# Kernel tuning notes

Hardware: AMD Instinct MI355X
Metric: run time of the kernel (lower is better)

The kernel has to match this reference:

```python
import jax, jax.numpy as jnp
import numpy as np

B, S, DM = 2, 2048, 2048
H, KV, HD = 32, 8, 64
ROPE_BASE = 10000.0


def rotate_half(x):
    x1, x2 = jnp.split(x, 2, axis=-1)
    return jnp.concatenate([-x2, x1], axis=-1)


def setup_inputs() -> dict:
    key = jax.random.key(0)
    ks = jax.random.split(key, 8)
    hidden_states = jax.random.normal(ks[0], (B, S, DM), dtype=jnp.float32)
    attention_mask = jnp.ones((B, S), dtype=jnp.int32)
    # RoPE tables: inv_freq over half the head dim, duplicated (HF-style)
    inv_freq = 1.0 / (ROPE_BASE ** (jnp.arange(0, HD, 2, dtype=jnp.float32) / HD))
    pos = jnp.arange(S, dtype=jnp.float32)
    freqs = pos[:, None] * inv_freq[None, :]            # [S, HD/2]
    emb = jnp.concatenate([freqs, freqs], axis=-1)      # [S, HD]
    cos = jnp.broadcast_to(jnp.cos(emb)[None], (B, S, HD))
    sin = jnp.broadcast_to(jnp.sin(emb)[None], (B, S, HD))
    sc = 1.0 / np.sqrt(DM)
    W_q = jax.random.normal(ks[1], (DM, H * HD), dtype=jnp.float32) * sc
    W_k = jax.random.normal(ks[2], (DM, KV * HD), dtype=jnp.float32) * sc
    W_v = jax.random.normal(ks[3], (DM, KV * HD), dtype=jnp.float32) * sc
    b_v = jax.random.normal(ks[4], (KV * HD,), dtype=jnp.float32) * 0.01
    W_o = jax.random.normal(ks[5], (H * HD, DM), dtype=jnp.float32) * sc
    b_o = jax.random.normal(ks[6], (DM,), dtype=jnp.float32) * 0.01
    return {"hidden_states": hidden_states, "attention_mask": attention_mask,
            "cos": cos, "sin": sin, "W_q": W_q, "W_k": W_k, "W_v": W_v,
            "b_v": b_v, "W_o": W_o, "b_o": b_o}


def reference(hidden_states, attention_mask, cos, sin, W_q, W_k, W_v, b_v, W_o, b_o):
    b, s, _ = hidden_states.shape
    q = hidden_states @ W_q                       # [B,S,H*HD]
    k = hidden_states @ W_k                       # [B,S,KV*HD]
    v = hidden_states @ W_v + b_v                 # [B,S,KV*HD]
    q = q.reshape(b, s, H, HD).transpose(0, 2, 1, 3)    # [B,H,S,HD]
    k = k.reshape(b, s, KV, HD).transpose(0, 2, 1, 3)   # [B,KV,S,HD]
    v = v.reshape(b, s, KV, HD).transpose(0, 2, 1, 3)
    c = cos[:, None]                              # [B,1,S,HD]
    sn = sin[:, None]
    q = q * c + rotate_half(q) * sn
    k = k * c + rotate_half(k) * sn
    groups = H // KV
    k = jnp.repeat(k, groups, axis=1)             # [B,H,S,HD]
    v = jnp.repeat(v, groups, axis=1)
    A = jnp.einsum('bhqd,bhkd->bhqk', q, k) / np.sqrt(HD).astype(np.float32)
    neg_inf = jnp.float32(-jnp.inf)
    causal = jnp.triu(jnp.full((s, s), neg_inf, dtype=jnp.float32), k=1)[None, None]
    mask = jnp.where(attention_mask[:, None, None, :] == 0, neg_inf, causal)
    A = jax.nn.softmax(A + mask, axis=-1)
    o = jnp.einsum('bhqk,bhkd->bhqd', A, v)
    o = o.transpose(0, 2, 1, 3).reshape(b, s, H * HD)
    return o @ W_o + b_o
```

## Files before the change

### kernel.cpp

```cpp
#include <hip/hip_runtime.h>
#include <hip/hip_bf16.h>

#define Bb 2
#define Ss 2048
#define DMD 2048
#define Hh 32
#define KVh 8
#define HD 64

using bf16 = __hip_bfloat16;
typedef __attribute__((ext_vector_type(8))) short short8;
typedef __attribute__((ext_vector_type(4))) float floatx4;

__device__ inline float tof(const bf16 x) { return __bfloat162float(x); }
__device__ inline void stor(float* p, float v) { *p = v; }
__device__ inline void stor(bf16* p, float v) { *p = __float2bfloat16(v); }
__device__ inline short bf16bits(float v) {
    union { bf16 h; short s; } cv; cv.h = __float2bfloat16(v); return cv.s;
}

__device__ inline void gl_lds16(const bf16* g, bf16* l) {
    __builtin_amdgcn_global_load_lds(
        (const __attribute__((address_space(1))) unsigned int*)g,
        (__attribute__((address_space(3))) unsigned int*)l, 16, 0, 0);
}

__global__ __launch_bounds__(256) void cvt_bf16_kernel(
    const float* __restrict__ in, bf16* __restrict__ out, int total8)
{
    const int i = blockIdx.x * 256 + threadIdx.x;
    if (i >= total8) return;
    const float4 a = ((const float4*)in)[2 * i];
    const float4 b = ((const float4*)in)[2 * i + 1];
    short8 r;
    r[0] = bf16bits(a.x); r[1] = bf16bits(a.y); r[2] = bf16bits(a.z); r[3] = bf16bits(a.w);
    r[4] = bf16bits(b.x); r[5] = bf16bits(b.y); r[6] = bf16bits(b.z); r[7] = bf16bits(b.w);
    ((short8*)out)[i] = r;
}

__global__ __launch_bounds__(256) void cvtT_kernel(
    const float* __restrict__ W, bf16* __restrict__ Wt,
    int N, int K, int rowOff)
{
    __shared__ float t[32][33];
    const int n0 = blockIdx.x * 32;
    const int k0 = blockIdx.y * 32;
    const int tx = threadIdx.x & 31, ty = threadIdx.x >> 5;
    #pragma unroll
    for (int r = 0; r < 32; r += 8)
        t[ty + r][tx] = W[(size_t)(k0 + ty + r) * N + n0 + tx];
    __syncthreads();
    #pragma unroll
    for (int r = 0; r < 32; r += 8)
        Wt[(size_t)(rowOff + n0 + ty + r) * K + k0 + tx] =
            __float2bfloat16(t[tx][ty + r]);
}

template <int EPI>
__global__ __launch_bounds__(256) void gemm_bt(
    const bf16* __restrict__ A, const bf16* __restrict__ Bt,
    const float* __restrict__ bias,
    bf16* __restrict__ Yq, bf16* __restrict__ Yk, bf16* __restrict__ Yv,
    float* __restrict__ Yo, int M, int N, int K)
{
    __shared__ bf16 As[128 * 32];
    __shared__ bf16 Bs[128 * 32];

    const int tid  = threadIdx.x;
    const int wave = tid >> 6, lane = tid & 63;
    const int lid  = lane & 15, quad = lane >> 4;
    const int wr = (wave >> 1) * 64, wc = (wave & 1) * 64;
    const size_t bm = (size_t)blockIdx.y * 128, bn = (size_t)blockIdx.x * 128;

    floatx4 acc[4][4];
    #pragma unroll
    for (int i = 0; i < 4; ++i)
        #pragma unroll
        for (int j = 0; j < 4; ++j)
            acc[i][j] = (floatx4){0.f, 0.f, 0.f, 0.f};

    for (int k0 = 0; k0 < K; k0 += 32) {
        #pragma unroll
        for (int i = 0; i < 2; ++i) {
            const int c   = wave * 128 + i * 64 + lane;
            const int row = c >> 2, col = (c & 3) * 8;
            gl_lds16(A  + (bm + row) * (size_t)K + k0 + col,
                     &As[(wave * 128 + i * 64) * 8]);
            gl_lds16(Bt + (bn + row) * (size_t)K + k0 + col,
                     &Bs[(wave * 128 + i * 64) * 8]);
        }
        __syncthreads();

        short8 af[4], bfr[4];
        #pragma unroll
        for (int i = 0; i < 4; ++i)
            af[i] = *(const short8*)&As[(wr + i * 16 + lid) * 32 + quad * 8];
        #pragma unroll
        for (int j = 0; j < 4; ++j)
            bfr[j] = *(const short8*)&Bs[(wc + j * 16 + lid) * 32 + quad * 8];
        #pragma unroll
        for (int i = 0; i < 4; ++i)
            #pragma unroll
            for (int j = 0; j < 4; ++j)
                acc[i][j] = __builtin_amdgcn_mfma_f32_16x16x32_bf16(
                    af[i], bfr[j], acc[i][j], 0, 0, 0);
        __syncthreads();
    }

    #pragma unroll
    for (int i = 0; i < 4; ++i) {
        const int gm0 = (int)bm + wr + i * 16 + quad * 4;
        #pragma unroll
        for (int j = 0; j < 4; ++j) {
            const int gn = (int)bn + wc + j * 16 + lid;
            #pragma unroll
            for (int r = 0; r < 4; ++r) {
                float v = acc[i][j][r];
                const int gm = gm0 + r;
                if (EPI == 0) {
                    if (gn < Hh * HD) {
                        stor(&Yq[(size_t)gm * (Hh * HD) + gn], v);
                    } else if (gn < Hh * HD + KVh * HD) {
                        stor(&Yk[(size_t)gm * (KVh * HD) + (gn - Hh * HD)], v);
                    } else {
                        const int c = gn - (Hh * HD + KVh * HD);
                        v += bias[c];
                        const int kvh = c >> 6, dd = c & 63;
                        const int bbi = gm >> 11, s = gm & (Ss - 1);
                        stor(&Yv[(((size_t)bbi * KVh + kvh) * HD + dd) * Ss + s], v);
                    }
                } else {
                    Yo[(size_t)gm * N + gn] = v + bias[gn];
                }
            }
        }
    }
}

__global__ void rope_kernel(bf16* __restrict__ buf,
                            const float* __restrict__ cosb,
                            const float* __restrict__ sinb,
                            int nheads, int total, float scale)
{
    int idx = blockIdx.x * blockDim.x + threadIdx.x;
    if (idx >= total) return;
    int d = idx & 31;
    int h = (idx >> 5) % nheads;
    int bs = idx / (32 * nheads);
    bf16* row = buf + ((size_t)bs * nheads + h) * HD;
    float x1 = tof(row[d]), x2 = tof(row[d + 32]);
    float c1 = cosb[(size_t)bs * HD + d];
    float s1 = sinb[(size_t)bs * HD + d];
    float c2 = cosb[(size_t)bs * HD + d + 32];
    float s2 = sinb[(size_t)bs * HD + d + 32];
    stor(&row[d],      (x1 * c1 - x2 * s1) * scale);
    stor(&row[d + 32], (x2 * c2 + x1 * s2) * scale);
}

template <bool CAUSAL>
__device__ inline void fattn_tile(
    const int k0, const int m0,
    const bf16* __restrict__ kBase, const bf16* __restrict__ vBase,
    const int* __restrict__ mBase,
    const short8 qf0[2], const short8 qf1[2],
    floatx4 o[2][4], float lsum[2][4],
    short (*pw)[16][72],
    const int lid, const int quad)
{
    const size_t kStride = (size_t)KVh * HD;

    short8 kb0[4], kb1[4];
    #pragma unroll
    for (int nt = 0; nt < 4; ++nt) {
        const bf16* kr = kBase + (size_t)(k0 + nt * 16 + lid) * kStride + quad * 8;
        kb0[nt] = *(const short8*)(kr);
        kb1[nt] = *(const short8*)(kr + 32);
    }
    floatx4 s[2][4];
    __builtin_amdgcn_s_setprio(1);
    #pragma unroll
    for (int nt = 0; nt < 4; ++nt)
        #pragma unroll
        for (int g = 0; g < 2; ++g) {
            floatx4 c = (floatx4){0.f, 0.f, 0.f, 0.f};
            c = __builtin_amdgcn_mfma_f32_16x16x32_bf16(qf0[g], kb0[nt], c, 0, 0, 0);
            c = __builtin_amdgcn_mfma_f32_16x16x32_bf16(qf1[g], kb1[nt], c, 0, 0, 0);
            s[g][nt] = c;
        }
    __builtin_amdgcn_s_setprio(0);

    short8 vb0[4], vb1[4];
    #pragma unroll
    for (int nt = 0; nt < 4; ++nt) {
        const bf16* vr = vBase + (size_t)(nt * 16 + lid) * Ss + k0 + quad * 8;
        vb0[nt] = *(const short8*)(vr);
        vb1[nt] = *(const short8*)(vr + 32);
    }

    #pragma unroll
    for (int nt = 0; nt < 4; ++nt) {
        const int col = k0 + nt * 16 + lid;
        const int mk  = mBase[col];
        #pragma unroll
        for (int g = 0; g < 2; ++g) {
            const int mr0 = m0 + g * 16 + quad * 4;
            #pragma unroll
            for (int rr = 0; rr < 4; ++rr) {
                float p;
                if (CAUSAL)
                    p = (mk == 0 || col > mr0 + rr) ? 0.f : __expf(s[g][nt][rr]);
                else
                    p = (mk == 0) ? 0.f : __expf(s[g][nt][rr]);
                s[g][nt][rr] = p;
                lsum[g][rr] += p;
            }
        }
    }

    #pragma unroll
    for (int g = 0; g < 2; ++g)
        #pragma unroll
        for (int nt = 0; nt < 4; ++nt)
            #pragma unroll
            for (int rr = 0; rr < 4; ++rr)
                pw[g][quad * 4 + rr][nt * 16 + lid] = bf16bits(s[g][nt][rr]);
    short8 pf0[2], pf1[2];
    #pragma unroll
    for (int g = 0; g < 2; ++g) {
        pf0[g] = *(const short8*)&pw[g][lid][quad * 8];
        pf1[g] = *(const short8*)&pw[g][lid][32 + quad * 8];
    }

    __builtin_amdgcn_s_setprio(1);
    #pragma unroll
    for (int nt = 0; nt < 4; ++nt)
        #pragma unroll
        for (int g = 0; g < 2; ++g) {
            o[g][nt] = __builtin_amdgcn_mfma_f32_16x16x32_bf16(
                pf0[g], vb0[nt], o[g][nt], 0, 0, 0);
            o[g][nt] = __builtin_amdgcn_mfma_f32_16x16x32_bf16(
                pf1[g], vb1[nt], o[g][nt], 0, 0, 0);
        }
    __builtin_amdgcn_s_setprio(0);
}

__global__ __launch_bounds__(256) void fattn_kernel(
    bf16* __restrict__ QO, const bf16* __restrict__ Kb,
    const bf16* __restrict__ Vt, const int* __restrict__ mask)
{
    const int bid    = blockIdx.x;
    const int kvh    = bid & 7;
    const int rest   = bid >> 3;
    const int qbslot = rest >> 3;
    const int bh     = rest & 7;
    const int hg     = bh & 3;
    const int b      = bh >> 2;
    const int qb     = 15 - qbslot;
    const int h      = kvh * 4 + hg;

    const int tid  = threadIdx.x;
    const int wave = tid >> 6;
    const int lane = tid & 63;
    const int lid  = lane & 15;
    const int quad = lane >> 4;

    const int qw = qb * 4 + wave;
    const int m0 = qw * 32;
    const int nfull = qw >> 1;

    __shared__ short pLds[4][2][16][72];

    const size_t kStride = (size_t)KVh * HD;
    const bf16* kBase = Kb + ((size_t)b * Ss) * kStride + (size_t)kvh * HD;
    const bf16* vBase = Vt + ((size_t)(b * KVh + kvh) * HD) * Ss;
    const int*  mBase = mask + b * Ss;

    short8 qf0[2], qf1[2];
    #pragma unroll
    for (int g = 0; g < 2; ++g) {
        const bf16* qb_ = QO + ((size_t)(b * Ss + m0 + g * 16 + lid) * Hh + h) * HD
                        + quad * 8;
        qf0[g] = *(const short8*)(qb_);
        qf1[g] = *(const short8*)(qb_ + 32);
    }

    floatx4 o[2][4];
    float lsum[2][4];
    #pragma unroll
    for (int g = 0; g < 2; ++g) {
        #pragma unroll
        for (int nt = 0; nt < 4; ++nt) o[g][nt] = (floatx4){0.f, 0.f, 0.f, 0.f};
        #pragma unroll
        for (int rr = 0; rr < 4; ++rr) lsum[g][rr] = 0.f;
    }

    for (int kt = 0; kt < nfull; ++kt)
        fattn_tile<false>(kt * 64, m0, kBase, vBase, mBase,
                          qf0, qf1, o, lsum, pLds[wave], lid, quad);
    fattn_tile<true>(nfull * 64, m0, kBase, vBase, mBase,
                     qf0, qf1, o, lsum, pLds[wave], lid, quad);

    #pragma unroll
    for (int g = 0; g < 2; ++g)
        #pragma unroll
        for (int rr = 0; rr < 4; ++rr) {
            float rs = lsum[g][rr];
            rs += __shfl_xor(rs, 1);
            rs += __shfl_xor(rs, 2);
            rs += __shfl_xor(rs, 4);
            rs += __shfl_xor(rs, 8);
            const float inv = 1.f / rs;
            const int m = m0 + g * 16 + quad * 4 + rr;
            bf16* orow = QO + ((size_t)(b * Ss + m) * Hh + h) * HD;
            #pragma unroll
            for (int nt = 0; nt < 4; ++nt)
                stor(&orow[nt * 16 + lid], o[g][nt][rr] * inv);
        }
}

extern "C" void kernel_launch(void* const* d_in, const int* in_sizes, int n_in,
                              void* d_out, int out_size, void* d_ws, size_t ws_size,
                              hipStream_t stream)
{
    const float* hs   = (const float*)d_in[0];
    const int*   mask = (const int*)d_in[1];
    const float* cosb = (const float*)d_in[2];
    const float* sinb = (const float*)d_in[3];
    const float* Wq   = (const float*)d_in[4];
    const float* Wk   = (const float*)d_in[5];
    const float* Wv   = (const float*)d_in[6];
    const float* bv   = (const float*)d_in[7];
    const float* Wo   = (const float*)d_in[8];
    const float* bo   = (const float*)d_in[9];
    float* out = (float*)d_out;

    const int M = Bb * Ss;

    bf16* QO    = (bf16*)d_ws;
    bf16* Wqkvt = QO + (size_t)M * (Hh * HD);
    bf16* Wot   = Wqkvt + (size_t)3072 * DMD;

    bf16* Kb  = (bf16*)d_out;
    bf16* Vt  = Kb + (size_t)M * (KVh * HD);
    bf16* Abf = Vt + (size_t)M * (KVh * HD);

    dim3 blk(256);

    const int total8 = M * DMD / 8;
    cvt_bf16_kernel<<<(total8 + 255) / 256, blk, 0, stream>>>(hs, Abf, total8);
    cvtT_kernel<<<dim3((Hh * HD) / 32, DMD / 32), blk, 0, stream>>>(
        Wq, Wqkvt, Hh * HD, DMD, 0);
    cvtT_kernel<<<dim3((KVh * HD) / 32, DMD / 32), blk, 0, stream>>>(
        Wk, Wqkvt, KVh * HD, DMD, Hh * HD);
    cvtT_kernel<<<dim3((KVh * HD) / 32, DMD / 32), blk, 0, stream>>>(
        Wv, Wqkvt, KVh * HD, DMD, Hh * HD + KVh * HD);
    cvtT_kernel<<<dim3(DMD / 32, DMD / 32), blk, 0, stream>>>(
        Wo, Wot, DMD, DMD, 0);

    gemm_bt<0><<<dim3(3072 / 128, M / 128), blk, 0, stream>>>(
        Abf, Wqkvt, bv, QO, Kb, Vt, nullptr, M, 3072, DMD);

    int totq = M * Hh * 32, totk = M * KVh * 32;
    rope_kernel<<<(totq + 255) / 256, blk, 0, stream>>>(QO, cosb, sinb, Hh, totq, 0.125f);
    rope_kernel<<<(totk + 255) / 256, blk, 0, stream>>>(Kb, cosb, sinb, KVh, totk, 1.0f);

    fattn_kernel<<<dim3(1024), blk, 0, stream>>>(QO, Kb, Vt, mask);

    gemm_bt<1><<<dim3(DMD / 128, M / 128), blk, 0, stream>>>(
        QO, Wot, bo, nullptr, nullptr, nullptr, out, M, DMD, DMD);
}
```

Baseline: 411.4 us.

## Compute transposed S tile and move P into MFMA layout with ds_permute instead of LDS

The QK^T MFMA now computes S transposed (K as the A operand), so each lane holds scores for one query row. The P tile is then converted with packed bf16 conversion and rearranged into the PV MFMA operand layout through ds_permute lane shuffles, replacing the LDS store/load round trip and the shared-memory buffer. Mask values are loaded as int4 vectors and row sums become per-lane, reducing the final shuffle count. The permute mapping is subtle and a mistake would silently corrupt results, and ds_permute still uses LDS hardware bandwidth.

```diff
diff --git a/kernel.cpp b/kernel.cpp
--- a/kernel.cpp
+++ b/kernel.cpp
@@ -17,6 +17,12 @@
 __device__ inline void stor(bf16* p, float v) { *p = __float2bfloat16(v); }
 __device__ inline short bf16bits(float v) {
     union { bf16 h; short s; } cv; cv.h = __float2bfloat16(v); return cv.s;
+}
+
+__device__ inline unsigned cvtpk_bf16(float lo, float hi) {
+    unsigned r;
+    asm("v_cvt_pk_bf16_f32 %0, %1, %2" : "=v"(r) : "v"(lo), "v"(hi));
+    return r;
 }
 
 __device__ inline void gl_lds16(const bf16* g, bf16* l) {
@@ -158,90 +164,96 @@
 }
 
 template <bool CAUSAL>
-__device__ inline void fattn_tile(
+__device__ __forceinline__ void fattn_tile(
     const int k0, const int m0,
     const bf16* __restrict__ kBase, const bf16* __restrict__ vBase,
     const int* __restrict__ mBase,
     const short8 qf0[2], const short8 qf1[2],
-    floatx4 o[2][4], float lsum[2][4],
-    short (*pw)[16][72],
-    const int lid, const int quad)
+    floatx4 o[2][4], float lsum[2],
+    const int lid, const int quad,
+    const int dstA[2], const int dstB[2])
 {
     const size_t kStride = (size_t)KVh * HD;
 
-    short8 kb0[4], kb1[4];
+    short8 ka0[4], ka1[4];
     #pragma unroll
     for (int nt = 0; nt < 4; ++nt) {
         const bf16* kr = kBase + (size_t)(k0 + nt * 16 + lid) * kStride + quad * 8;
-        kb0[nt] = *(const short8*)(kr);
-        kb1[nt] = *(const short8*)(kr + 32);
-    }
-    floatx4 s[2][4];
+        ka0[nt] = *(const short8*)(kr);
+        ka1[nt] = *(const short8*)(kr + 32);
+    }
+
+    floatx4 st[2][4];
     __builtin_amdgcn_s_setprio(1);
     #pragma unroll
     for (int nt = 0; nt < 4; ++nt)
         #pragma unroll
         for (int g = 0; g < 2; ++g) {
             floatx4 c = (floatx4){0.f, 0.f, 0.f, 0.f};
-            c = __builtin_amdgcn_mfma_f32_16x16x32_bf16(qf0[g], kb0[nt], c, 0, 0, 0);
-            c = __builtin_amdgcn_mfma_f32_16x16x32_bf16(qf1[g], kb1[nt], c, 0, 0, 0);
-            s[g][nt] = c;
+            c = __builtin_amdgcn_mfma_f32_16x16x32_bf16(ka0[nt], qf0[g], c, 0, 0, 0);
+            c = __builtin_amdgcn_mfma_f32_16x16x32_bf16(ka1[nt], qf1[g], c, 0, 0, 0);
+            st[g][nt] = c;
         }
     __builtin_amdgcn_s_setprio(0);
 
-    short8 vb0[4], vb1[4];
+    short8 vb[4][2];
+    #pragma unroll
+    for (int dt = 0; dt < 4; ++dt)
+        #pragma unroll
+        for (int ch = 0; ch < 2; ++ch)
+            vb[dt][ch] = *(const short8*)(vBase + (size_t)(dt * 16 + lid) * Ss
+                                          + k0 + ch * 32 + quad * 8);
+
+    int mk[4][4];
     #pragma unroll
     for (int nt = 0; nt < 4; ++nt) {
-        const bf16* vr = vBase + (size_t)(nt * 16 + lid) * Ss + k0 + quad * 8;
-        vb0[nt] = *(const short8*)(vr);
-        vb1[nt] = *(const short8*)(vr + 32);
-    }
-
-    #pragma unroll
-    for (int nt = 0; nt < 4; ++nt) {
-        const int col = k0 + nt * 16 + lid;
-        const int mk  = mBase[col];
-        #pragma unroll
-        for (int g = 0; g < 2; ++g) {
-            const int mr0 = m0 + g * 16 + quad * 4;
-            #pragma unroll
-            for (int rr = 0; rr < 4; ++rr) {
-                float p;
-                if (CAUSAL)
-                    p = (mk == 0 || col > mr0 + rr) ? 0.f : __expf(s[g][nt][rr]);
-                else
-                    p = (mk == 0) ? 0.f : __expf(s[g][nt][rr]);
-                s[g][nt][rr] = p;
-                lsum[g][rr] += p;
+        const int4 m4 = *(const int4*)(mBase + k0 + nt * 16 + quad * 4);
+        mk[nt][0] = m4.x; mk[nt][1] = m4.y; mk[nt][2] = m4.z; mk[nt][3] = m4.w;
+    }
+
+    #pragma unroll
+    for (int g = 0; g < 2; ++g) {
+        const int qrow = m0 + g * 16 + lid;
+        #pragma unroll
+        for (int nt = 0; nt < 4; ++nt)
+            #pragma unroll
+            for (int r = 0; r < 4; ++r) {
+                const int kcol = k0 + nt * 16 + quad * 4 + r;
+                const float p = (mk[nt][r] == 0 || (CAUSAL && kcol > qrow))
+                              ? 0.f : __expf(st[g][nt][r]);
+                st[g][nt][r] = p;
+                lsum[g] += p;
             }
-        }
-    }
-
-    #pragma unroll
-    for (int g = 0; g < 2; ++g)
-        #pragma unroll
-        for (int nt = 0; nt < 4; ++nt)
-            #pragma unroll
-            for (int rr = 0; rr < 4; ++rr)
-                pw[g][quad * 4 + rr][nt * 16 + lid] = bf16bits(s[g][nt][rr]);
-    short8 pf0[2], pf1[2];
+    }
+
     #pragma unroll
     for (int g = 0; g < 2; ++g) {
-        pf0[g] = *(const short8*)&pw[g][lid][quad * 8];
-        pf1[g] = *(const short8*)&pw[g][lid][32 + quad * 8];
-    }
-
-    __builtin_amdgcn_s_setprio(1);
-    #pragma unroll
-    for (int nt = 0; nt < 4; ++nt)
-        #pragma unroll
-        for (int g = 0; g < 2; ++g) {
-            o[g][nt] = __builtin_amdgcn_mfma_f32_16x16x32_bf16(
-                pf0[g], vb0[nt], o[g][nt], 0, 0, 0);
-            o[g][nt] = __builtin_amdgcn_mfma_f32_16x16x32_bf16(
-                pf1[g], vb1[nt], o[g][nt], 0, 0, 0);
-        }
-    __builtin_amdgcn_s_setprio(0);
+        unsigned w[4][2];
+        #pragma unroll
+        for (int nt = 0; nt < 4; ++nt) {
+            w[nt][0] = cvtpk_bf16(st[g][nt][0], st[g][nt][1]);
+            w[nt][1] = cvtpk_bf16(st[g][nt][2], st[g][nt][3]);
+        }
+        union { unsigned u[4]; short8 s; } pf[2];
+        #pragma unroll
+        for (int c = 0; c < 2; ++c)
+            #pragma unroll
+            for (int m = 0; m < 4; ++m) {
+                const int p = m >> 1, j = m & 1;
+                const int v1 = __builtin_amdgcn_ds_permute(dstA[p], (int)w[2 * c][j]);
+                const int v2 = __builtin_amdgcn_ds_permute(dstB[p], (int)w[2 * c + 1][j]);
+                pf[c].u[m] = (quad < 2) ? v1 : v2;
+            }
+        __builtin_amdgcn_s_setprio(1);
+        #pragma unroll
+        for (int dt = 0; dt < 4; ++dt) {
+            o[g][dt] = __builtin_amdgcn_mfma_f32_16x16x32_bf16(
+                pf[0].s, vb[dt][0], o[g][dt], 0, 0, 0);
+            o[g][dt] = __builtin_amdgcn_mfma_f32_16x16x32_bf16(
+                pf[1].s, vb[dt][1], o[g][dt], 0, 0, 0);
+        }
+        __builtin_amdgcn_s_setprio(0);
+    }
 }
 
 __global__ __launch_bounds__(256) void fattn_kernel(
@@ -268,7 +280,13 @@
     const int m0 = qw * 32;
     const int nfull = qw >> 1;
 
-    __shared__ short pLds[4][2][16][72];
+    int dstA[2], dstB[2];
+    #pragma unroll
+    for (int p = 0; p < 2; ++p) {
+        const bool on = ((quad & 1) == p);
+        dstA[p] = 4 * (on ? ((quad >> 1) * 16 + lid) : (32 + (quad >> 1) * 16 + lid));
+        dstB[p] = 4 * (on ? (32 + (quad >> 1) * 16 + lid) : ((quad >> 1) * 16 + lid));
+    }
 
     const size_t kStride = (size_t)KVh * HD;
     const bf16* kBase = Kb + ((size_t)b * Ss) * kStride + (size_t)kvh * HD;
@@ -285,37 +303,34 @@
     }
 
     floatx4 o[2][4];
-    float lsum[2][4];
-    #pragma unroll
-    for (int g = 0; g < 2; ++g) {
-        #pragma unroll
-        for (int nt = 0; nt < 4; ++nt) o[g][nt] = (floatx4){0.f, 0.f, 0.f, 0.f};
-        #pragma unroll
-        for (int rr = 0; rr < 4; ++rr) lsum[g][rr] = 0.f;
-    }
+    float lsum[2] = {0.f, 0.f};
+    #pragma unroll
+    for (int g = 0; g < 2; ++g)
+        #pragma unroll
+        for (int dt = 0; dt < 4; ++dt) o[g][dt] = (floatx4){0.f, 0.f, 0.f, 0.f};
 
     for (int kt = 0; kt < nfull; ++kt)
         fattn_tile<false>(kt * 64, m0, kBase, vBase, mBase,
-                          qf0, qf1, o, lsum, pLds[wave], lid, quad);
+                          qf0, qf1, o, lsum, lid, quad, dstA, dstB);
     fattn_tile<true>(nfull * 64, m0, kBase, vBase, mBase,
-                     qf0, qf1, o, lsum, pLds[wave], lid, quad);
-
-    #pragma unroll
-    for (int g = 0; g < 2; ++g)
-        #pragma unroll
-        for (int rr = 0; rr < 4; ++rr) {
-            float rs = lsum[g][rr];
-            rs += __shfl_xor(rs, 1);
-            rs += __shfl_xor(rs, 2);
-            rs += __shfl_xor(rs, 4);
-            rs += __shfl_xor(rs, 8);
-            const float inv = 1.f / rs;
-            const int m = m0 + g * 16 + quad * 4 + rr;
+                     qf0, qf1, o, lsum, lid, quad, dstA, dstB);
+
+    #pragma unroll
+    for (int g = 0; g < 2; ++g) {
+        float rs = lsum[g];
+        rs += __shfl_xor(rs, 16);
+        rs += __shfl_xor(rs, 32);
+        const float inv = 1.f / rs;
+        #pragma unroll
+        for (int reg = 0; reg < 4; ++reg) {
+            const float invr = __shfl(inv, quad * 4 + reg);
+            const int m = m0 + g * 16 + quad * 4 + reg;
             bf16* orow = QO + ((size_t)(b * Ss + m) * Hh + h) * HD;
             #pragma unroll
-            for (int nt = 0; nt < 4; ++nt)
-                stor(&orow[nt * 16 + lid], o[g][nt][rr] * inv);
-        }
+            for (int dt = 0; dt < 4; ++dt)
+                stor(&orow[dt * 16 + lid], o[g][dt][reg] * invr);
+        }
+    }
 }
 
 extern "C" void kernel_launch(void* const* d_in, const int* in_sizes, int n_in,
```

New measurement: 421.3 us. +2.4%, slower.
